# Kernel optimization log

Hardware: AMD Instinct MI355X
Metric: run time of the kernel (lower is better)

The kernel has to match this reference:

```python
import jax, jax.numpy as jnp
import numpy as np

B, N, M, D = 8, 512, 64, 128
H = 64  # mlp_hidden_dim


def setup_inputs() -> dict:
    key = jax.random.key(0)
    ks = jax.random.split(key, 10)
    op_emb = jax.random.normal(ks[0], (B, N, D), dtype=jnp.float32)
    machine_emb = jax.random.normal(ks[1], (B, M, D), dtype=jnp.float32)
    edge_emb = jax.random.normal(ks[2], (B, N, M, D), dtype=jnp.float32)
    action_mask = jax.random.randint(ks[3], (B, N, M), 0, 2) > 0
    s1 = 1.0 / np.sqrt(3 * D)
    s2 = 1.0 / np.sqrt(H)
    W1 = jax.random.uniform(ks[4], (3 * D, H), jnp.float32, -s1, s1)
    b1 = jax.random.uniform(ks[5], (H,), jnp.float32, -s1, s1)
    W2 = jax.random.uniform(ks[6], (H, H), jnp.float32, -s2, s2)
    b2 = jax.random.uniform(ks[7], (H,), jnp.float32, -s2, s2)
    W3 = jax.random.uniform(ks[8], (H, 1), jnp.float32, -s2, s2)
    b3 = jax.random.uniform(ks[9], (1,), jnp.float32, -s2, s2)
    return {"op_emb": op_emb, "machine_emb": machine_emb, "edge_emb": edge_emb,
            "action_mask": action_mask,
            "W1": W1, "b1": b1, "W2": W2, "b2": b2, "W3": W3, "b3": b3}


def reference(op_emb, machine_emb, edge_emb, action_mask, W1, b1, W2, b2, W3, b3):
    # Split first linear over the three concat chunks to avoid materializing
    # the (B,N,M,3D) concat tensor (same math as cat -> Linear).
    Wo, Wm, We = W1[:D], W1[D:2 * D], W1[2 * D:]
    h = (jnp.einsum('bnd,dh->bnh', op_emb, Wo)[:, :, None, :]
         + jnp.einsum('bmd,dh->bmh', machine_emb, Wm)[:, None, :, :]
         + jnp.einsum('bnmd,dh->bnmh', edge_emb, We) + b1)  # (B,N,M,H)
    h = jax.nn.relu(h)
    h = jax.nn.relu(h @ W2 + b2)
    scores = (h @ W3 + b3)[..., 0]  # (B,N,M)
    scores = jnp.where(action_mask, scores, -jnp.inf)
    return jax.nn.log_softmax(scores.reshape(B, N * M), axis=-1)
```

## Files before the change

### kernel.cpp

```cpp
#include <hip/hip_runtime.h>
#include <math.h>

#define Bb 8
#define Nn 512
#define Mm 64
#define Dd 128
#define Hh 64
#define Gg 4
#define NEG_BIG (-1.0e30f)

typedef __bf16 bf16x8 __attribute__((ext_vector_type(8)));
typedef float  f32x4  __attribute__((ext_vector_type(4)));

#define WS_WEB   0u
#define WS_W2B   16384u
#define WS_CWS   24576u
#define WS_AOP   155648u
#define WS_SCORE 1204224u
#define WS_PART  2252800u

__global__ __launch_bounds__(256) void prep_kernel(
    const float* __restrict__ W1, const float* __restrict__ W2,
    const float* __restrict__ op_emb, const float* __restrict__ machine_emb,
    const float* __restrict__ b1, char* __restrict__ ws)
{
    if (blockIdx.x < 48) {
        __bf16* WeB = (__bf16*)(ws + WS_WEB);
        __bf16* W2B = (__bf16*)(ws + WS_W2B);
        int idx = blockIdx.x * 256 + threadIdx.x;
        if (idx < 8192) {
            int fid = idx >> 9, rem = idx & 511;
            int lane = rem >> 3, j = rem & 7;
            int t = fid >> 2, ks = fid & 3;
            int q = lane >> 4, ln = lane & 15;
            int d = ks * 32 + q * 8 + j;
            int h = t * 16 + ln;
            WeB[idx] = (__bf16)W1[(size_t)(2 * Dd + d) * Hh + h];
        } else {
            int i2 = idx - 8192;
            int fid = i2 >> 9, rem = i2 & 511;
            int lane = rem >> 3, j = rem & 7;
            int t = fid >> 1, ks = fid & 1;
            int q = lane >> 4, ln = lane & 15;
            int k = ks * 32 + q * 8 + j;
            int h = t * 16 + ln;
            W2B[i2] = (__bf16)W2[(size_t)k * Hh + h];
        }
        return;
    }
    float* Cws = (float*)(ws + WS_CWS);
    float* Aop = (float*)(ws + WS_AOP);
    const int bid = (blockIdx.x - 48) * 4 + (threadIdx.x >> 6);
    const int h = threadIdx.x & 63;
    if (bid < Bb * Mm) {
        const float* mg = machine_emb + (size_t)bid * Dd;
        const float* Wm = W1 + (size_t)Dd * Hh;
        float acc = b1[h];
#pragma unroll 8
        for (int d = 0; d < Dd; ++d) acc = fmaf(mg[d], Wm[d * Hh + h], acc);
        Cws[(size_t)bid * Hh + h] = acc;
    } else {
        const int bn = bid - Bb * Mm;
        const float* og = op_emb + (size_t)bn * Dd;
        float acc = 0.f;
#pragma unroll 8
        for (int d = 0; d < Dd; ++d) acc = fmaf(og[d], W1[d * Hh + h], acc);
        Aop[(size_t)bn * Hh + h] = acc;
    }
}

__global__ __launch_bounds__(256, 4) void main_kernel(
    const float* __restrict__ edge_emb, const int* __restrict__ mask,
    const float* __restrict__ b2, const float* __restrict__ W3,
    const float* __restrict__ b3, char* __restrict__ ws)
{
    __shared__ __bf16 sH1[Mm * 72];

    const __bf16* WeB = (const __bf16*)(ws + WS_WEB);
    const __bf16* W2B = (const __bf16*)(ws + WS_W2B);
    const float*  Cws = (const float*)(ws + WS_CWS);
    const float*  Aop = (const float*)(ws + WS_AOP);
    float* scores     = (float*)(ws + WS_SCORE);

    const int tid  = threadIdx.x;
    const int lane = tid & 63;
    const int w    = tid >> 6;
    const int q    = lane >> 4;
    const int ln   = lane & 15;
    const int bn0  = blockIdx.x * Gg;
    const int b    = bn0 >> 9;
    const int mrow = w * 16 + ln;

    float cv[16];
#pragma unroll
    for (int t = 0; t < 4; ++t)
#pragma unroll
        for (int r = 0; r < 4; ++r)
            cv[t * 4 + r] = Cws[((size_t)b * Mm + w * 16 + q * 4 + r) * Hh + t * 16 + ln];
    float b2v[4], w3v[4];
#pragma unroll
    for (int t = 0; t < 4; ++t) { b2v[t] = b2[t * 16 + ln]; w3v[t] = W3[t * 16 + ln]; }
    const float bias3 = b3[0];

    float4 raw[8]; float aopv[4]; int4 mk = {0, 0, 0, 0};
    {
        const float* Eg = edge_emb + (size_t)bn0 * (Mm * Dd) + mrow * Dd + q * 8;
#pragma unroll
        for (int ks = 0; ks < 4; ++ks) {
            raw[2 * ks]     = *(const float4*)&Eg[ks * 32];
            raw[2 * ks + 1] = *(const float4*)&Eg[ks * 32 + 4];
        }
#pragma unroll
        for (int t = 0; t < 4; ++t) aopv[t] = Aop[(size_t)bn0 * Hh + t * 16 + ln];
        if (ln == 0) mk = *(const int4*)&mask[(size_t)bn0 * Mm + w * 16 + q * 4];
    }

#pragma unroll
    for (int g = 0; g < Gg; ++g) {
        const int bn = bn0 + g;

        bf16x8 af[4];
#pragma unroll
        for (int ks = 0; ks < 4; ++ks) {
            float4 lo = raw[2 * ks], hi = raw[2 * ks + 1];
            bf16x8 a;
            a[0] = (__bf16)lo.x; a[1] = (__bf16)lo.y; a[2] = (__bf16)lo.z; a[3] = (__bf16)lo.w;
            a[4] = (__bf16)hi.x; a[5] = (__bf16)hi.y; a[6] = (__bf16)hi.z; a[7] = (__bf16)hi.w;
            af[ks] = a;
        }
        float naop[4] = {};
        int4  nmk = {0, 0, 0, 0};
        if (g + 1 < Gg) {
            const float* Eg = edge_emb + (size_t)(bn + 1) * (Mm * Dd) + mrow * Dd + q * 8;
#pragma unroll
            for (int ks = 0; ks < 4; ++ks) {
                raw[2 * ks]     = *(const float4*)&Eg[ks * 32];
                raw[2 * ks + 1] = *(const float4*)&Eg[ks * 32 + 4];
            }
#pragma unroll
            for (int t = 0; t < 4; ++t) naop[t] = Aop[(size_t)(bn + 1) * Hh + t * 16 + ln];
            if (ln == 0) nmk = *(const int4*)&mask[(size_t)(bn + 1) * Mm + w * 16 + q * 4];
        }

        f32x4 acc[4];
#pragma unroll
        for (int t = 0; t < 4; ++t)
#pragma unroll
            for (int r = 0; r < 4; ++r)
                acc[t][r] = aopv[t] + cv[t * 4 + r];

#pragma unroll
        for (int t = 0; t < 4; ++t)
#pragma unroll
            for (int ks = 0; ks < 4; ++ks) {
                bf16x8 bfr = *(const bf16x8*)&WeB[((t * 4 + ks) * 64 + lane) * 8];
                acc[t] = __builtin_amdgcn_mfma_f32_16x16x32_bf16(af[ks], bfr, acc[t], 0, 0, 0);
            }

#pragma unroll
        for (int t = 0; t < 4; ++t)
#pragma unroll
            for (int r = 0; r < 4; ++r)
                sH1[(w * 16 + q * 4 + r) * 72 + t * 16 + ln] =
                    (__bf16)fmaxf(acc[t][r], 0.f);

        bf16x8 a2[2];
#pragma unroll
        for (int ks = 0; ks < 2; ++ks)
            a2[ks] = *(const bf16x8*)&sH1[(w * 16 + ln) * 72 + ks * 32 + q * 8];
        f32x4 c2[4];
#pragma unroll
        for (int t = 0; t < 4; ++t) c2[t] = (f32x4){0.f, 0.f, 0.f, 0.f};
#pragma unroll
        for (int t = 0; t < 4; ++t)
#pragma unroll
            for (int ks = 0; ks < 2; ++ks) {
                bf16x8 bfr = *(const bf16x8*)&W2B[((t * 2 + ks) * 64 + lane) * 8];
                c2[t] = __builtin_amdgcn_mfma_f32_16x16x32_bf16(a2[ks], bfr, c2[t], 0, 0, 0);
            }

        float p[4] = {0.f, 0.f, 0.f, 0.f};
#pragma unroll
        for (int t = 0; t < 4; ++t)
#pragma unroll
            for (int r = 0; r < 4; ++r)
                p[r] += fmaxf(c2[t][r] + b2v[t], 0.f) * w3v[t];
#pragma unroll
        for (int r = 0; r < 4; ++r) {
            p[r] += __shfl_xor(p[r], 1, 64);
            p[r] += __shfl_xor(p[r], 2, 64);
            p[r] += __shfl_xor(p[r], 4, 64);
            p[r] += __shfl_xor(p[r], 8, 64);
        }
        if (ln == 0) {
            float4 o;
            o.x = mk.x ? (p[0] + bias3) : NEG_BIG;
            o.y = mk.y ? (p[1] + bias3) : NEG_BIG;
            o.z = mk.z ? (p[2] + bias3) : NEG_BIG;
            o.w = mk.w ? (p[3] + bias3) : NEG_BIG;
            *(float4*)&scores[(size_t)bn * Mm + w * 16 + q * 4] = o;
        }
#pragma unroll
        for (int t = 0; t < 4; ++t) aopv[t] = naop[t];
        mk = nmk;
    }
}

__global__ __launch_bounds__(256) void lsm_part_kernel(char* __restrict__ ws)
{
    const float* s = (const float*)(ws + WS_SCORE);
    float* part = (float*)(ws + WS_PART);
    __shared__ float sm[4], ss[4];
    const int c = blockIdx.x;
    const int tid = threadIdx.x;
    const int lane = tid & 63, wv = tid >> 6;

    float2 v = *(const float2*)&s[(size_t)c * 512 + tid * 2];
    float m = fmaxf(v.x, v.y);
#pragma unroll
    for (int off = 1; off < 64; off <<= 1) m = fmaxf(m, __shfl_xor(m, off, 64));
    if (lane == 0) sm[wv] = m;
    __syncthreads();
    float gm = fmaxf(fmaxf(sm[0], sm[1]), fmaxf(sm[2], sm[3]));

    float e = expf(v.x - gm) + expf(v.y - gm);
#pragma unroll
    for (int off = 1; off < 64; off <<= 1) e += __shfl_xor(e, off, 64);
    if (lane == 0) ss[wv] = e;
    __syncthreads();
    if (tid == 0) {
        float2 o; o.x = gm; o.y = ss[0] + ss[1] + ss[2] + ss[3];
        *(float2*)&part[c * 2] = o;
    }
}

__global__ __launch_bounds__(256) void lsm_apply_kernel(
    const char* __restrict__ ws, float* __restrict__ out)
{
    const float4* s4 = (const float4*)(ws + WS_SCORE);
    const float* part = (const float*)(ws + WS_PART);
    __shared__ float sCC;
    const int tid = threadIdx.x;
    const int b = blockIdx.x >> 5;
    if (tid < 64) {
        float2 p = *(const float2*)&part[(b * 64 + tid) * 2];
        float gm = p.x;
#pragma unroll
        for (int off = 1; off < 64; off <<= 1) gm = fmaxf(gm, __shfl_xor(gm, off, 64));
        float l = p.y * expf(p.x - gm);
#pragma unroll
        for (int off = 1; off < 64; off <<= 1) l += __shfl_xor(l, off, 64);
        if (tid == 0) sCC = gm + logf(l);
    }
    __syncthreads();
    const float c = sCC;
    const int i = blockIdx.x * 256 + tid;
    float4 v = s4[i];
    v.x -= c; v.y -= c; v.z -= c; v.w -= c;
    ((float4*)out)[i] = v;
}

extern "C" void kernel_launch(void* const* d_in, const int* in_sizes, int n_in,
                              void* d_out, int out_size, void* d_ws, size_t ws_size,
                              hipStream_t stream)
{
    const float* op_emb      = (const float*)d_in[0];
    const float* machine_emb = (const float*)d_in[1];
    const float* edge_emb    = (const float*)d_in[2];
    const int*   mask        = (const int*)  d_in[3];
    const float* W1 = (const float*)d_in[4];
    const float* b1 = (const float*)d_in[5];
    const float* W2 = (const float*)d_in[6];
    const float* b2 = (const float*)d_in[7];
    const float* W3 = (const float*)d_in[8];
    const float* b3 = (const float*)d_in[9];
    char* ws = (char*)d_ws;

    prep_kernel<<<48 + 1152, 256, 0, stream>>>(W1, W2, op_emb, machine_emb, b1, ws);
    main_kernel<<<(Bb * Nn) / Gg, 256, 0, stream>>>(edge_emb, mask, b2, W3, b3, ws);
    lsm_part_kernel<<<512, 256, 0, stream>>>(ws);
    lsm_apply_kernel<<<256, 256, 0, stream>>>(ws, (float*)d_out);
}
```

Baseline: 267.3 us.

## Stream edge tiles into LDS with async double-buffered loads and larger groups

Edge embedding rows are now fetched with global_load_lds into a per-wave double buffer, two steps ahead, with explicit vmcnt waits. Each block handles 16 ops instead of 4. The layer-1 and layer-2 weight fragments are held in registers, and the machine projection, op projection and mask are staged once in LDS, with the machine projection stored in a pre-swizzled layout. The aim is to hide global latency and remove redundant weight loads, at the cost of far fewer blocks and waves per CU.

Measured after the change: 233.5 us. 12.7% less time.

```diff
diff --git a/kernel.cpp b/kernel.cpp
--- a/kernel.cpp
+++ b/kernel.cpp
@@ -6,7 +6,7 @@
 #define Mm 64
 #define Dd 128
 #define Hh 64
-#define Gg 4
+#define Gg 16
 #define NEG_BIG (-1.0e30f)
 
 typedef __bf16 bf16x8 __attribute__((ext_vector_type(8)));
@@ -14,10 +14,14 @@
 
 #define WS_WEB   0u
 #define WS_W2B   16384u
-#define WS_CWS   24576u
+#define WS_CWSF  24576u
 #define WS_AOP   155648u
 #define WS_SCORE 1204224u
 #define WS_PART  2252800u
+
+#define GLOAD_LDS(gp, lp) __builtin_amdgcn_global_load_lds( \
+    (const __attribute__((address_space(1))) void*)(gp),    \
+    (__attribute__((address_space(3))) void*)(lp), 16, 0, 0)
 
 __global__ __launch_bounds__(256) void prep_kernel(
     const float* __restrict__ W1, const float* __restrict__ W2,
@@ -48,8 +52,8 @@
         }
         return;
     }
-    float* Cws = (float*)(ws + WS_CWS);
-    float* Aop = (float*)(ws + WS_AOP);
+    float* CwsF = (float*)(ws + WS_CWSF);
+    float* Aop  = (float*)(ws + WS_AOP);
     const int bid = (blockIdx.x - 48) * 4 + (threadIdx.x >> 6);
     const int h = threadIdx.x & 63;
     if (bid < Bb * Mm) {
@@ -58,7 +62,10 @@
         float acc = b1[h];
 #pragma unroll 8
         for (int d = 0; d < Dd; ++d) acc = fmaf(mg[d], Wm[d * Hh + h], acc);
-        Cws[(size_t)bid * Hh + h] = acc;
+        int b = bid >> 6, m = bid & 63;
+        int wq = m >> 4, q = (m >> 2) & 3, r = m & 3;
+        int t = h >> 4, ln = h & 15;
+        CwsF[((((b * 4 + wq) * 4 + t) * 64) + (q * 16 + ln)) * 4 + r] = acc;
     } else {
         const int bn = bid - Bb * Mm;
         const float* og = op_emb + (size_t)bn * Dd;
@@ -69,18 +76,18 @@
     }
 }
 
-__global__ __launch_bounds__(256, 4) void main_kernel(
+__global__ __launch_bounds__(256, 1) void main_kernel(
     const float* __restrict__ edge_emb, const int* __restrict__ mask,
     const float* __restrict__ b2, const float* __restrict__ W3,
     const float* __restrict__ b3, char* __restrict__ ws)
 {
+    __shared__ float  sEdge[4 * 2 * 2048];
+    __shared__ float  sCwsF[4096];
+    __shared__ float  sAop[Gg * Hh];
+    __shared__ int    sMask[Gg * Mm];
     __shared__ __bf16 sH1[Mm * 72];
 
-    const __bf16* WeB = (const __bf16*)(ws + WS_WEB);
-    const __bf16* W2B = (const __bf16*)(ws + WS_W2B);
-    const float*  Cws = (const float*)(ws + WS_CWS);
-    const float*  Aop = (const float*)(ws + WS_AOP);
-    float* scores     = (float*)(ws + WS_SCORE);
+    float* scores = (float*)(ws + WS_SCORE);
 
     const int tid  = threadIdx.x;
     const int lane = tid & 63;
@@ -89,73 +96,94 @@
     const int ln   = lane & 15;
     const int bn0  = blockIdx.x * Gg;
     const int b    = bn0 >> 9;
-    const int mrow = w * 16 + ln;
-
-    float cv[16];
-#pragma unroll
-    for (int t = 0; t < 4; ++t)
-#pragma unroll
-        for (int r = 0; r < 4; ++r)
-            cv[t * 4 + r] = Cws[((size_t)b * Mm + w * 16 + q * 4 + r) * Hh + t * 16 + ln];
+    const int wu   = __builtin_amdgcn_readfirstlane(w);
+
+    const float* ebase = edge_emb + ((size_t)bn0 * Mm + w * 16 + ln) * Dd + q * 8;
+
+    {
+        float* d0 = &sEdge[(wu * 2 + 0) * 2048];
+        float* d1 = &sEdge[(wu * 2 + 1) * 2048];
+#pragma unroll
+        for (int s = 0; s < 8; ++s)
+            GLOAD_LDS(ebase + (s >> 1) * 32 + (s & 1) * 4, d0 + s * 256);
+#pragma unroll
+        for (int s = 0; s < 8; ++s)
+            GLOAD_LDS(ebase + 8192 + (s >> 1) * 32 + (s & 1) * 4, d1 + s * 256);
+    }
+
+    {
+        const f32x4* s3 = (const f32x4*)(ws + WS_CWSF) + (size_t)b * 1024;
+        f32x4* d3 = (f32x4*)sCwsF;
+#pragma unroll
+        for (int i = 0; i < 4; ++i) d3[tid + 256 * i] = s3[tid + 256 * i];
+        ((f32x4*)sAop)[tid]  = ((const f32x4*)((ws + WS_AOP)))[(size_t)bn0 * 16 + tid];
+        ((int4*)sMask)[tid]  = ((const int4*)mask)[(size_t)bn0 * 16 + tid];
+    }
+
+    bf16x8 weF[16], w2F[8];
+    {
+        const bf16x8* WeB = (const bf16x8*)(ws + WS_WEB);
+        const bf16x8* W2B = (const bf16x8*)(ws + WS_W2B);
+#pragma unroll
+        for (int f = 0; f < 16; ++f) weF[f] = WeB[f * 64 + lane];
+#pragma unroll
+        for (int f = 0; f < 8; ++f)  w2F[f] = W2B[f * 64 + lane];
+    }
+
     float b2v[4], w3v[4];
 #pragma unroll
     for (int t = 0; t < 4; ++t) { b2v[t] = b2[t * 16 + ln]; w3v[t] = W3[t * 16 + ln]; }
     const float bias3 = b3[0];
 
-    float4 raw[8]; float aopv[4]; int4 mk = {0, 0, 0, 0};
-    {
-        const float* Eg = edge_emb + (size_t)bn0 * (Mm * Dd) + mrow * Dd + q * 8;
+    __syncthreads();
+
+#pragma unroll
+    for (int g = 0; g < Gg; ++g) {
+        const int buf = g & 1;
+        const float* ldsrd = &sEdge[(wu * 2 + buf) * 2048];
+
+        if (g == Gg - 1) __builtin_amdgcn_s_waitcnt(0x0F70);
+        else             __builtin_amdgcn_s_waitcnt(0x0F78);
+
+        f32x4 lo[4], hi[4];
 #pragma unroll
         for (int ks = 0; ks < 4; ++ks) {
-            raw[2 * ks]     = *(const float4*)&Eg[ks * 32];
-            raw[2 * ks + 1] = *(const float4*)&Eg[ks * 32 + 4];
-        }
-#pragma unroll
-        for (int t = 0; t < 4; ++t) aopv[t] = Aop[(size_t)bn0 * Hh + t * 16 + ln];
-        if (ln == 0) mk = *(const int4*)&mask[(size_t)bn0 * Mm + w * 16 + q * 4];
-    }
-
-#pragma unroll
-    for (int g = 0; g < Gg; ++g) {
-        const int bn = bn0 + g;
-
+            lo[ks] = *(const f32x4*)&ldsrd[(ks * 2 + 0) * 256 + lane * 4];
+            hi[ks] = *(const f32x4*)&ldsrd[(ks * 2 + 1) * 256 + lane * 4];
+        }
         bf16x8 af[4];
 #pragma unroll
         for (int ks = 0; ks < 4; ++ks) {
-            float4 lo = raw[2 * ks], hi = raw[2 * ks + 1];
             bf16x8 a;
-            a[0] = (__bf16)lo.x; a[1] = (__bf16)lo.y; a[2] = (__bf16)lo.z; a[3] = (__bf16)lo.w;
-            a[4] = (__bf16)hi.x; a[5] = (__bf16)hi.y; a[6] = (__bf16)hi.z; a[7] = (__bf16)hi.w;
+            a[0] = (__bf16)lo[ks][0]; a[1] = (__bf16)lo[ks][1];
+            a[2] = (__bf16)lo[ks][2]; a[3] = (__bf16)lo[ks][3];
+            a[4] = (__bf16)hi[ks][0]; a[5] = (__bf16)hi[ks][1];
+            a[6] = (__bf16)hi[ks][2]; a[7] = (__bf16)hi[ks][3];
             af[ks] = a;
         }
-        float naop[4] = {};
-        int4  nmk = {0, 0, 0, 0};
-        if (g + 1 < Gg) {
-            const float* Eg = edge_emb + (size_t)(bn + 1) * (Mm * Dd) + mrow * Dd + q * 8;
-#pragma unroll
-            for (int ks = 0; ks < 4; ++ks) {
-                raw[2 * ks]     = *(const float4*)&Eg[ks * 32];
-                raw[2 * ks + 1] = *(const float4*)&Eg[ks * 32 + 4];
-            }
-#pragma unroll
-            for (int t = 0; t < 4; ++t) naop[t] = Aop[(size_t)(bn + 1) * Hh + t * 16 + ln];
-            if (ln == 0) nmk = *(const int4*)&mask[(size_t)(bn + 1) * Mm + w * 16 + q * 4];
+
+        if (g + 2 < Gg) {
+            float* dst = &sEdge[(wu * 2 + buf) * 2048];
+            const float* src = ebase + (size_t)(g + 2) * 8192;
+#pragma unroll
+            for (int s = 0; s < 8; ++s)
+                GLOAD_LDS(src + (s >> 1) * 32 + (s & 1) * 4, dst + s * 256);
         }
 
         f32x4 acc[4];
 #pragma unroll
+        for (int t = 0; t < 4; ++t) {
+            f32x4 cv4 = *(const f32x4*)&sCwsF[((w * 4 + t) * 64 + lane) * 4];
+            float av = sAop[g * Hh + t * 16 + ln];
+            acc[t][0] = cv4[0] + av; acc[t][1] = cv4[1] + av;
+            acc[t][2] = cv4[2] + av; acc[t][3] = cv4[3] + av;
+        }
+
+#pragma unroll
         for (int t = 0; t < 4; ++t)
 #pragma unroll
-            for (int r = 0; r < 4; ++r)
-                acc[t][r] = aopv[t] + cv[t * 4 + r];
-
-#pragma unroll
-        for (int t = 0; t < 4; ++t)
-#pragma unroll
-            for (int ks = 0; ks < 4; ++ks) {
-                bf16x8 bfr = *(const bf16x8*)&WeB[((t * 4 + ks) * 64 + lane) * 8];
-                acc[t] = __builtin_amdgcn_mfma_f32_16x16x32_bf16(af[ks], bfr, acc[t], 0, 0, 0);
-            }
+            for (int ks = 0; ks < 4; ++ks)
+                acc[t] = __builtin_amdgcn_mfma_f32_16x16x32_bf16(af[ks], weF[t * 4 + ks], acc[t], 0, 0, 0);
 
 #pragma unroll
         for (int t = 0; t < 4; ++t)
@@ -174,10 +202,8 @@
 #pragma unroll
         for (int t = 0; t < 4; ++t)
 #pragma unroll
-            for (int ks = 0; ks < 2; ++ks) {
-                bf16x8 bfr = *(const bf16x8*)&W2B[((t * 2 + ks) * 64 + lane) * 8];
-                c2[t] = __builtin_amdgcn_mfma_f32_16x16x32_bf16(a2[ks], bfr, c2[t], 0, 0, 0);
-            }
+            for (int ks = 0; ks < 2; ++ks)
+                c2[t] = __builtin_amdgcn_mfma_f32_16x16x32_bf16(a2[ks], w2F[t * 2 + ks], c2[t], 0, 0, 0);
 
         float p[4] = {0.f, 0.f, 0.f, 0.f};
 #pragma unroll
@@ -193,16 +219,15 @@
             p[r] += __shfl_xor(p[r], 8, 64);
         }
         if (ln == 0) {
+            const int m0 = w * 16 + q * 4;
+            const int* mrow = &sMask[g * Mm + m0];
             float4 o;
-            o.x = mk.x ? (p[0] + bias3) : NEG_BIG;
-            o.y = mk.y ? (p[1] + bias3) : NEG_BIG;
-            o.z = mk.z ? (p[2] + bias3) : NEG_BIG;
-            o.w = mk.w ? (p[3] + bias3) : NEG_BIG;
-            *(float4*)&scores[(size_t)bn * Mm + w * 16 + q * 4] = o;
-        }
-#pragma unroll
-        for (int t = 0; t < 4; ++t) aopv[t] = naop[t];
-        mk = nmk;
+            o.x = mrow[0] ? (p[0] + bias3) : NEG_BIG;
+            o.y = mrow[1] ? (p[1] + bias3) : NEG_BIG;
+            o.z = mrow[2] ? (p[2] + bias3) : NEG_BIG;
+            o.w = mrow[3] ? (p[3] + bias3) : NEG_BIG;
+            *(float4*)&scores[(size_t)(bn0 + g) * Mm + m0] = o;
+        }
     }
 }
 
```
